# Kernel optimization log

Hardware: AMD Instinct MI355X
Metric: run time of the kernel (lower is better)

## Reference

```python
import jax, jax.numpy as jnp
import numpy as np

N_SRC, N_DST, E, D, H = 100000, 10000, 320000, 128, 128
LN_EPS = 1e-5


def setup_inputs() -> dict:
    key = jax.random.key(0)
    ks = jax.random.split(key, 12)
    h_src = jax.random.normal(ks[0], (N_SRC, D), jnp.float32)
    h_dst = jax.random.normal(ks[1], (N_DST, D), jnp.float32)
    s_emb = jax.random.normal(ks[2], (N_DST, D), jnp.float32)
    edge_weight = jax.random.uniform(ks[3], (E,), jnp.float32)
    src_idx = jax.random.randint(ks[4], (E,), 0, N_SRC)
    dst_idx = jnp.sort(jax.random.randint(ks[5], (E,), 0, N_DST))
    # session_attention: Linear(2D->H, no bias) -> tanh -> Linear(H->1, no bias)
    W1 = jax.random.normal(ks[6], (2 * D, H), jnp.float32) / np.sqrt(2 * D)
    w2 = jax.random.normal(ks[7], (H,), jnp.float32) / np.sqrt(H)
    # output_proj: Linear(2D->D) with bias
    Wo = jax.random.normal(ks[8], (2 * D, D), jnp.float32) / np.sqrt(2 * D)
    bo = jnp.zeros((D,), jnp.float32)
    gamma = jnp.ones((D,), jnp.float32)
    beta = jnp.zeros((D,), jnp.float32)
    return {"h_src": h_src, "h_dst": h_dst, "s_emb": s_emb,
            "edge_weight": edge_weight, "src_idx": src_idx, "dst_idx": dst_idx,
            "W1": W1, "w2": w2, "Wo": Wo, "bo": bo, "gamma": gamma, "beta": beta}


def reference(h_src, h_dst, s_emb, edge_weight, src_idx, dst_idx, W1, w2, Wo, bo, gamma, beta):
    d = h_src.shape[1]
    # concat([h_src[src], s_emb[dst]]) @ W1 == h_src[src] @ W1[:d] + s_emb[dst] @ W1[d:]
    # project per-node first (cheaper than per-edge concat matmul)
    p_src = h_src @ W1[:d]          # [N_src, H]
    p_dst = s_emb @ W1[d:]          # [N_dst, H]
    raw = jnp.tanh(p_src[src_idx] + p_dst[dst_idx]) @ w2   # [E]
    raw = raw * edge_weight
    # edge_softmax: segment softmax over incoming edges of each dst node
    seg_max = jax.ops.segment_max(raw, dst_idx, num_segments=h_dst.shape[0])
    seg_max = jnp.where(jnp.isfinite(seg_max), seg_max, 0.0)  # handle degree-0 dsts
    ex = jnp.exp(raw - seg_max[dst_idx])
    den = jax.ops.segment_sum(ex, dst_idx, num_segments=h_dst.shape[0])
    attn = ex / den[dst_idx]                                 # [E]
    # u_mul_e + sum: weighted gather-scatter aggregation
    h_global = jax.ops.segment_sum(h_src[src_idx] * attn[:, None], dst_idx,
                                   num_segments=h_dst.shape[0])  # [N_dst, D]
    # output_proj on concat([h_dst, h_global])
    out = h_dst @ Wo[:d] + h_global @ Wo[d:] + bo
    # residual + layer norm (dropout = identity in eval)
    x = h_dst + out
    mu = jnp.mean(x, axis=-1, keepdims=True)
    var = jnp.mean((x - mu) ** 2, axis=-1, keepdims=True)
    y = (x - mu) / jnp.sqrt(var + LN_EPS) * gamma + beta
    return (y, attn[:, None])
```

## Files before the change

### kernel.cpp

```cpp
#include <hip/hip_runtime.h>
#include <math.h>

#define D128 128
#define SCAP 1024

typedef unsigned int uint32;
typedef unsigned short ushort_t;
typedef short bf16x8 __attribute__((ext_vector_type(8)));
typedef float f32x4 __attribute__((ext_vector_type(4)));

__device__ __forceinline__ ushort_t bf16_of(float x) {
  uint32 u = __float_as_uint(x);
  return (ushort_t)((u + 0x7fffu + ((u >> 16) & 1u)) >> 16);
}
__device__ __forceinline__ uint32 pack_bf2(float x, float y) {
  uint32 bx = __float_as_uint(x);
  uint32 by = __float_as_uint(y);
  bx = (bx + 0x7fffu + ((bx >> 16) & 1u)) >> 16;
  by = (by + 0x7fffu + ((by >> 16) & 1u)) & 0xffff0000u;
  return bx | by;
}
__device__ __forceinline__ float bf_lo(uint32 u) { return __uint_as_float(u << 16); }
__device__ __forceinline__ float bf_hi(uint32 u) { return __uint_as_float(u & 0xffff0000u); }

__device__ __forceinline__ float fast_tanh(float x) {
  float e = __expf(2.0f * x);
  float r = __builtin_amdgcn_rcpf(1.0f + e);
  return fmaf(-2.0f, r, 1.0f);
}

__global__ __launch_bounds__(256) void prep_all(
    const float* __restrict__ h_src, const float* __restrict__ s_emb,
    const float* __restrict__ h_dst,
    const float* __restrict__ W1, const float* __restrict__ Wo,
    const int* __restrict__ dst_idx,
    uint32* __restrict__ h_src_bf, uint32* __restrict__ s_emb_bf,
    uint32* __restrict__ h_dst_bf,
    ushort_t* __restrict__ Wfrag, ushort_t* __restrict__ Wo_frag,
    int* __restrict__ off,
    int n_src_el, int n_dst_el, int E, int N, int nb_conv) {
  const int b = blockIdx.x;
  const int tid = threadIdx.x;
  if (b < nb_conv) {
    int i = (b * 256 + tid) * 8;
    const int n_tot_el = n_src_el + 2 * n_dst_el;
    if (i >= n_tot_el) return;
    const float* src;
    uint32* dst;
    if (i < n_src_el) { src = h_src + i; dst = h_src_bf + (i >> 1); }
    else if (i < n_src_el + n_dst_el) {
      src = s_emb + (i - n_src_el); dst = s_emb_bf + ((i - n_src_el) >> 1);
    } else {
      src = h_dst + (i - n_src_el - n_dst_el);
      dst = h_dst_bf + ((i - n_src_el - n_dst_el) >> 1);
    }
    float4 a = *(const float4*)src;
    float4 c = *(const float4*)(src + 4);
    uint4 p;
    p.x = pack_bf2(a.x, a.y);
    p.y = pack_bf2(a.z, a.w);
    p.z = pack_bf2(c.x, c.y);
    p.w = pack_bf2(c.z, c.w);
    *(uint4*)dst = p;
  } else if (b < nb_conv + 16) {
    int t = (b - nb_conv) * 256 + tid;
    int lane = t & 63;
    int kc = (t >> 6) & 3;
    int nt = (t >> 8) & 7;
    int h = (t >> 11) & 1;
    int m = lane & 15;
    int quad = lane >> 4;
    int krow = h * D128 + kc * 32 + quad * 8;
    int ncol = nt * 16 + m;
    ushort_t fr[8];
#pragma unroll
    for (int j = 0; j < 8; j++) fr[j] = bf16_of(W1[(size_t)(krow + j) * D128 + ncol]);
    *(uint4*)(Wfrag + (size_t)t * 8) = *(const uint4*)fr;
  } else if (b < nb_conv + 32) {
    int t = (b - nb_conv - 16) * 256 + tid;
    int lane = t & 63;
    int kc = (t >> 6) & 7;
    int nt = (t >> 9) & 7;
    int m = lane & 15;
    int quad = lane >> 4;
    int krow = kc * 32 + quad * 8;
    int ncol = nt * 16 + m;
    ushort_t fr[8];
#pragma unroll
    for (int j = 0; j < 8; j++) fr[j] = bf16_of(Wo[(size_t)(krow + j) * D128 + ncol]);
    *(uint4*)(Wo_frag + (size_t)t * 8) = *(const uint4*)fr;
  } else {
    int e = (b - nb_conv - 32) * 256 + tid;
    if (e >= E) return;
    int d = dst_idx[e];
    int dprev = (e == 0) ? -1 : dst_idx[e - 1];
    for (int v = dprev + 1; v <= d; v++) off[v] = e;
    if (e == E - 1) {
      for (int v = d + 1; v <= N; v++) off[v] = E;
    }
  }
}

__global__ __launch_bounds__(256) void gemm_mfma(
    const ushort_t* __restrict__ Xa, const ushort_t* __restrict__ Xb,
    const ushort_t* __restrict__ Wfrag,
    ushort_t* __restrict__ Pa, ushort_t* __restrict__ Pb,
    int Ma, int Mb, int nblk_a) {
  __shared__ ushort_t Ys[128][132];
  const int blk = blockIdx.x;
  const ushort_t* X;
  const bf16x8* Wf;
  ushort_t* P;
  int M, row0;
  if (blk < nblk_a) { X = Xa; P = Pa; Wf = (const bf16x8*)Wfrag;           M = Ma; row0 = blk * 128; }
  else              { X = Xb; P = Pb; Wf = (const bf16x8*)(Wfrag + 16384); M = Mb; row0 = (blk - nblk_a) * 128; }

  const int tid = threadIdx.x;
  const int wave = tid >> 6;
  const int lane = tid & 63;
  const int m = lane & 15;
  const int quad = lane >> 4;

  const int ra0 = min(row0 + wave * 32 + m, M - 1);
  const int ra1 = min(row0 + wave * 32 + 16 + m, M - 1);

  f32x4 acc[2][8];
#pragma unroll
  for (int st = 0; st < 2; st++)
#pragma unroll
    for (int nt = 0; nt < 8; nt++) acc[st][nt] = (f32x4){0.f, 0.f, 0.f, 0.f};

#pragma unroll
  for (int kc = 0; kc < 4; kc++) {
    bf16x8 a0 = *(const bf16x8*)(X + (size_t)ra0 * D128 + kc * 32 + quad * 8);
    bf16x8 a1 = *(const bf16x8*)(X + (size_t)ra1 * D128 + kc * 32 + quad * 8);
#pragma unroll
    for (int nt = 0; nt < 8; nt++) {
      bf16x8 bfr = Wf[(nt * 4 + kc) * 64 + lane];
      acc[0][nt] = __builtin_amdgcn_mfma_f32_16x16x32_bf16(a0, bfr, acc[0][nt], 0, 0, 0);
      acc[1][nt] = __builtin_amdgcn_mfma_f32_16x16x32_bf16(a1, bfr, acc[1][nt], 0, 0, 0);
    }
  }

#pragma unroll
  for (int st = 0; st < 2; st++)
#pragma unroll
    for (int nt = 0; nt < 8; nt++)
#pragma unroll
      for (int r = 0; r < 4; r++)
        Ys[wave * 32 + st * 16 + quad * 4 + r][nt * 16 + m] = bf16_of(acc[st][nt][r]);
  __syncthreads();

#pragma unroll
  for (int it = 0; it < 16; it++) {
    int f = tid + 256 * it;
    int row = f >> 5;
    int c = (f & 31) * 4;
    int grow = row0 + row;
    if (grow < M) {
      uint2 v = *(const uint2*)(&Ys[row][c]);
      *(uint2*)(P + (size_t)grow * D128 + c) = v;
    }
  }
}

__global__ __launch_bounds__(256) void attn_agg_kernel(
    const uint32* __restrict__ p_src_bf, const uint32* __restrict__ p_dst_bf,
    const float* __restrict__ w2, const float* __restrict__ ew,
    const int* __restrict__ src_idx, const int* __restrict__ off,
    const uint32* __restrict__ h_src_bf2,
    float* __restrict__ attn_out, uint32* __restrict__ h_glob_bf) {
  const int v = blockIdx.x;
  const int tid = threadIdx.x;
  const int lo = off[v], hi = off[v + 1];
  const int deg = hi - lo;
  const int sub = tid & 15;
  const int eg16 = tid >> 4;
  const int t2 = tid & 63;
  const int wv = tid >> 6;

  __shared__ float sw2[128];
  __shared__ uint32 spd[64];
  __shared__ float sred[4];
  __shared__ float sex[SCAP];
  __shared__ int ssrc[SCAP];
  __shared__ float sacc[4][128];

  if (tid < 128) sw2[tid] = w2[tid];
  if (tid < 64) spd[tid] = p_dst_bf[(size_t)v * 64 + tid];
  __syncthreads();

  float accx = 0.f, accy = 0.f;
  float inv;

  if (deg <= SCAP) {
    for (int base = 0; base < deg; base += 16) {
      int ei = base + eg16;
      float acc = 0.f;
      int s = 0;
      if (ei < deg) {
        int e = lo + ei;
        s = src_idx[e];
        uint4 us = *(const uint4*)(p_src_bf + (size_t)s * 64 + sub * 4);
        uint4 ud = *(const uint4*)(&spd[sub * 4]);
        float4 wA = *(const float4*)(&sw2[sub * 8]);
        float4 wB = *(const float4*)(&sw2[sub * 8 + 4]);
        acc = fast_tanh(bf_lo(us.x) + bf_lo(ud.x)) * wA.x;
        acc = fmaf(fast_tanh(bf_hi(us.x) + bf_hi(ud.x)), wA.y, acc);
        acc = fmaf(fast_tanh(bf_lo(us.y) + bf_lo(ud.y)), wA.z, acc);
        acc = fmaf(fast_tanh(bf_hi(us.y) + bf_hi(ud.y)), wA.w, acc);
        acc = fmaf(fast_tanh(bf_lo(us.z) + bf_lo(ud.z)), wB.x, acc);
        acc = fmaf(fast_tanh(bf_hi(us.z) + bf_hi(ud.z)), wB.y, acc);
        acc = fmaf(fast_tanh(bf_lo(us.w) + bf_lo(ud.w)), wB.z, acc);
        acc = fmaf(fast_tanh(bf_hi(us.w) + bf_hi(ud.w)), wB.w, acc);
      }
#pragma unroll
      for (int o = 1; o <= 8; o <<= 1) acc += __shfl_xor(acc, o, 64);
      if (ei < deg && sub == 0) { sex[ei] = acc * ew[lo + ei]; ssrc[ei] = s; }
    }
    const int pad = (deg + 7) & ~7;
    for (int i = deg + tid; i < pad; i += 256) { sex[i] = 0.f; ssrc[i] = 0; }
    __syncthreads();

    float dp = 0.f;
    for (int i = tid; i < deg; i += 256) {
      float ex = __expf(sex[i]);
      sex[i] = ex;
      dp += ex;
    }
#pragma unroll
    for (int o = 32; o >= 1; o >>= 1) dp += __shfl_xor(dp, o, 64);
    if (t2 == 0) sred[wv] = dp;
    __syncthreads();
    inv = (deg > 0) ? 1.0f / (((sred[0] + sred[1]) + (sred[2] + sred[3]))) : 0.0f;

    for (int i = tid; i < deg; i += 256) attn_out[lo + i] = sex[i] * inv;

    const int nb = (deg + 7) >> 3;
    for (int b = wv; b < nb; b += 4) {
      const int base = b * 8;
#pragma unroll
      for (int j = 0; j < 8; j++) {
        float ex = sex[base + j];
        int s = ssrc[base + j];
        uint32 u = h_src_bf2[(size_t)s * 64 + t2];
        accx = fmaf(ex, bf_lo(u), accx);
        accy = fmaf(ex, bf_hi(u), accy);
      }
    }
  } else {
    for (int base = 0; base < deg; base += 16) {
      int ei = base + eg16;
      float acc = 0.f;
      if (ei < deg) {
        int e = lo + ei;
        int s = src_idx[e];
        uint4 us = *(const uint4*)(p_src_bf + (size_t)s * 64 + sub * 4);
        uint4 ud = *(const uint4*)(&spd[sub * 4]);
        float4 wA = *(const float4*)(&sw2[sub * 8]);
        float4 wB = *(const float4*)(&sw2[sub * 8 + 4]);
        acc = fast_tanh(bf_lo(us.x) + bf_lo(ud.x)) * wA.x;
        acc = fmaf(fast_tanh(bf_hi(us.x) + bf_hi(ud.x)), wA.y, acc);
        acc = fmaf(fast_tanh(bf_lo(us.y) + bf_lo(ud.y)), wA.z, acc);
        acc = fmaf(fast_tanh(bf_hi(us.y) + bf_hi(ud.y)), wA.w, acc);
        acc = fmaf(fast_tanh(bf_lo(us.z) + bf_lo(ud.z)), wB.x, acc);
        acc = fmaf(fast_tanh(bf_hi(us.z) + bf_hi(ud.z)), wB.y, acc);
        acc = fmaf(fast_tanh(bf_lo(us.w) + bf_lo(ud.w)), wB.z, acc);
        acc = fmaf(fast_tanh(bf_hi(us.w) + bf_hi(ud.w)), wB.w, acc);
      }
#pragma unroll
      for (int o = 1; o <= 8; o <<= 1) acc += __shfl_xor(acc, o, 64);
      if (ei < deg && sub == 0) attn_out[lo + ei] = acc * ew[lo + ei];
    }
    __syncthreads();

    float dp = 0.f;
    for (int i = tid; i < deg; i += 256) dp += __expf(attn_out[lo + i]);
#pragma unroll
    for (int o = 32; o >= 1; o >>= 1) dp += __shfl_xor(dp, o, 64);
    if (t2 == 0) sred[wv] = dp;
    __syncthreads();
    inv = 1.0f / (((sred[0] + sred[1]) + (sred[2] + sred[3])));

    for (int w0 = 0; w0 < deg; w0 += SCAP) {
      const int wn = min(SCAP, deg - w0);
      __syncthreads();
      for (int i = tid; i < wn; i += 256) {
        float ex = __expf(attn_out[lo + w0 + i]);
        sex[i] = ex;
        ssrc[i] = src_idx[lo + w0 + i];
        attn_out[lo + w0 + i] = ex * inv;
      }
      const int padw = (wn + 7) & ~7;
      for (int i = wn + tid; i < padw; i += 256) { sex[i] = 0.f; ssrc[i] = 0; }
      __syncthreads();
      const int nb = (wn + 7) >> 3;
      for (int b = wv; b < nb; b += 4) {
        const int base = b * 8;
#pragma unroll
        for (int j = 0; j < 8; j++) {
          float ex = sex[base + j];
          int s = ssrc[base + j];
          uint32 u = h_src_bf2[(size_t)s * 64 + t2];
          accx = fmaf(ex, bf_lo(u), accx);
          accy = fmaf(ex, bf_hi(u), accy);
        }
      }
    }
  }

  sacc[wv][t2 * 2] = accx;
  sacc[wv][t2 * 2 + 1] = accy;
  __syncthreads();
  if (tid < 64) {
    float sx = (sacc[0][tid * 2] + sacc[1][tid * 2]) + (sacc[2][tid * 2] + sacc[3][tid * 2]);
    float sy = (sacc[0][tid * 2 + 1] + sacc[1][tid * 2 + 1]) +
               (sacc[2][tid * 2 + 1] + sacc[3][tid * 2 + 1]);
    h_glob_bf[(size_t)v * 64 + tid] = pack_bf2(sx * inv, sy * inv);
  }
}

__global__ __launch_bounds__(128) void out_mfma_ln(
    const ushort_t* __restrict__ h_dst_bf, const ushort_t* __restrict__ h_glob_bf,
    const ushort_t* __restrict__ Wo_frag,
    const float* __restrict__ h_dst, const float* __restrict__ bo,
    const float* __restrict__ gamma, const float* __restrict__ beta,
    float* __restrict__ y, int N) {
  __shared__ float sbo[128], sgam[128], sbet[128];
  const int tid = threadIdx.x;
  if (tid < 128) { sbo[tid] = bo[tid]; sgam[tid] = gamma[tid]; sbet[tid] = beta[tid]; }
  __syncthreads();

  const int w = tid >> 6;
  const int lane = tid & 63;
  const int m = lane & 15;
  const int quad = lane >> 4;
  const int row0 = blockIdx.x * 32 + w * 16;
  const int ra = min(row0 + m, N - 1);
  const bf16x8* Wf = (const bf16x8*)Wo_frag;

  f32x4 acc[8];
#pragma unroll
  for (int nt = 0; nt < 8; nt++) acc[nt] = (f32x4){0.f, 0.f, 0.f, 0.f};

#pragma unroll
  for (int kc = 0; kc < 8; kc++) {
    const ushort_t* X = (kc < 4) ? h_dst_bf : h_glob_bf;
    const int kk = kc & 3;
    bf16x8 a = *(const bf16x8*)(X + (size_t)ra * D128 + kk * 32 + quad * 8);
#pragma unroll
    for (int nt = 0; nt < 8; nt++) {
      bf16x8 bfr = Wf[(nt * 8 + kc) * 64 + lane];
      acc[nt] = __builtin_amdgcn_mfma_f32_16x16x32_bf16(a, bfr, acc[nt], 0, 0, 0);
    }
  }

#pragma unroll
  for (int r = 0; r < 4; r++) {
    const int grow = row0 + quad * 4 + r;
    const int gr = min(grow, N - 1);
    float x[8];
    float s1 = 0.f, s2 = 0.f;
#pragma unroll
    for (int nt = 0; nt < 8; nt++) {
      float hd = h_dst[(size_t)gr * D128 + nt * 16 + m];
      float xv = hd + acc[nt][r] + sbo[nt * 16 + m];
      x[nt] = xv;
      s1 += xv;
      s2 = fmaf(xv, xv, s2);
    }
#pragma unroll
    for (int o = 1; o <= 8; o <<= 1) {
      s1 += __shfl_xor(s1, o, 64);
      s2 += __shfl_xor(s2, o, 64);
    }
    float mu = s1 * (1.0f / 128.0f);
    float var = s2 * (1.0f / 128.0f) - mu * mu;
    float rstd = __builtin_amdgcn_rcpf(sqrtf(var + 1e-5f));
    if (grow < N) {
#pragma unroll
      for (int nt = 0; nt < 8; nt++) {
        int c = nt * 16 + m;
        y[(size_t)grow * D128 + c] = (x[nt] - mu) * rstd * sgam[c] + sbet[c];
      }
    }
  }
}

extern "C" void kernel_launch(void* const* d_in, const int* in_sizes, int n_in,
                              void* d_out, int out_size, void* d_ws, size_t ws_size,
                              hipStream_t stream) {
  const float* h_src = (const float*)d_in[0];
  const float* h_dst = (const float*)d_in[1];
  const float* s_emb = (const float*)d_in[2];
  const float* ew    = (const float*)d_in[3];
  const int* src_idx = (const int*)d_in[4];
  const int* dst_idx = (const int*)d_in[5];
  const float* W1    = (const float*)d_in[6];
  const float* w2    = (const float*)d_in[7];
  const float* Wo    = (const float*)d_in[8];
  const float* bo    = (const float*)d_in[9];
  const float* gamma = (const float*)d_in[10];
  const float* beta  = (const float*)d_in[11];

  const int N_src = in_sizes[0] / D128;
  const int N_dst = in_sizes[1] / D128;
  const int E = in_sizes[3];

  float* out_y = (float*)d_out;
  float* out_attn = out_y + (size_t)N_dst * D128;

  uint32* p_src_bf = (uint32*)d_ws;
  uint32* p_dst_bf = p_src_bf + (size_t)N_src * 64;
  uint32* h_src_bf = p_dst_bf + (size_t)N_dst * 64;
  uint32* h_dst_bf = h_src_bf + (size_t)N_src * 64;
  uint32* h_glob_bf = h_dst_bf + (size_t)N_dst * 64;
  uint32* s_emb_bf = h_glob_bf + (size_t)N_dst * 64;
  int* seg_off = (int*)(s_emb_bf + (size_t)N_dst * 64);
  ushort_t* Wfrag = (ushort_t*)(seg_off + N_dst + 1 + 3);
  ushort_t* Wo_frag = Wfrag + 32768;

  const int n_src_el = N_src * D128;
  const int n_dst_el = N_dst * D128;
  const int n_tot_el = n_src_el + 2 * n_dst_el;
  const int nblk_a = (N_src + 127) / 128;
  const int nblk_b = (N_dst + 127) / 128;
  const int nb_conv = (n_tot_el / 8 + 255) / 256;
  const int nb_seg = (E + 255) / 256;

  prep_all<<<nb_conv + 32 + nb_seg, 256, 0, stream>>>(
      h_src, s_emb, h_dst, W1, Wo, dst_idx,
      h_src_bf, s_emb_bf, h_dst_bf, Wfrag, Wo_frag, seg_off,
      n_src_el, n_dst_el, E, N_dst, nb_conv);
  gemm_mfma<<<nblk_a + nblk_b, 256, 0, stream>>>(
      (const ushort_t*)h_src_bf, (const ushort_t*)s_emb_bf, Wfrag,
      (ushort_t*)p_src_bf, (ushort_t*)p_dst_bf, N_src, N_dst, nblk_a);
  attn_agg_kernel<<<N_dst, 256, 0, stream>>>(
      p_src_bf, p_dst_bf, w2, ew, src_idx, seg_off, h_src_bf, out_attn, h_glob_bf);
  out_mfma_ln<<<(N_dst + 31) / 32, 128, 0, stream>>>(
      (const ushort_t*)h_dst_bf, (const ushort_t*)h_glob_bf, Wo_frag,
      h_dst, bo, gamma, beta, out_y, N_dst);
}
```

Baseline: 177.4 us.

## Map one wavefront per destination node in attention aggregation kernel

Changes the attention/aggregation kernel from one 256-thread block per destination node to one 64-lane wavefront per node, with four nodes per block. All block-level syncs and shared-memory cross-wave reductions are replaced by wave shuffles. The exp is fused into the score loop so the denominator accumulates without a separate pass. With average degree 32, most of a block's threads previously sat idle; the cost is a serial per-wave loop for high-degree nodes and load imbalance between waves in a block.

```diff
diff --git a/kernel.cpp b/kernel.cpp
--- a/kernel.cpp
+++ b/kernel.cpp
@@ -2,7 +2,7 @@
 #include <math.h>
 
 #define D128 128
-#define SCAP 1024
+#define SCAPW 256
 
 typedef unsigned int uint32;
 typedef unsigned short ushort_t;
@@ -169,42 +169,42 @@
     const float* __restrict__ w2, const float* __restrict__ ew,
     const int* __restrict__ src_idx, const int* __restrict__ off,
     const uint32* __restrict__ h_src_bf2,
-    float* __restrict__ attn_out, uint32* __restrict__ h_glob_bf) {
-  const int v = blockIdx.x;
+    float* __restrict__ attn_out, uint32* __restrict__ h_glob_bf, int N_dst) {
   const int tid = threadIdx.x;
+  const int wv = tid >> 6;
+  const int lane = tid & 63;
+  const int v = blockIdx.x * 4 + wv;
+
+  __shared__ float sw2[128];
+  __shared__ float sex[4][SCAPW];
+  __shared__ int ssrc[4][SCAPW];
+
+  if (tid < 128) sw2[tid] = w2[tid];
+  __syncthreads();
+  if (v >= N_dst) return;
+
   const int lo = off[v], hi = off[v + 1];
   const int deg = hi - lo;
-  const int sub = tid & 15;
-  const int eg16 = tid >> 4;
-  const int t2 = tid & 63;
-  const int wv = tid >> 6;
-
-  __shared__ float sw2[128];
-  __shared__ uint32 spd[64];
-  __shared__ float sred[4];
-  __shared__ float sex[SCAP];
-  __shared__ int ssrc[SCAP];
-  __shared__ float sacc[4][128];
-
-  if (tid < 128) sw2[tid] = w2[tid];
-  if (tid < 64) spd[tid] = p_dst_bf[(size_t)v * 64 + tid];
-  __syncthreads();
-
+  const int sub = lane & 15;
+  const int eg = lane >> 4;
+
+  uint4 ud = *(const uint4*)(p_dst_bf + (size_t)v * 64 + sub * 4);
+  float4 wA = *(const float4*)(&sw2[sub * 8]);
+  float4 wB = *(const float4*)(&sw2[sub * 8 + 4]);
+
+  float den = 0.f;
   float accx = 0.f, accy = 0.f;
-  float inv;
-
-  if (deg <= SCAP) {
-    for (int base = 0; base < deg; base += 16) {
-      int ei = base + eg16;
-      float acc = 0.f;
+
+  if (deg <= SCAPW) {
+    for (int base = 0; base < deg; base += 4) {
+      const int ei = base + eg;
+      float acc = 0.f, ewv = 0.f;
       int s = 0;
       if (ei < deg) {
-        int e = lo + ei;
+        const int e = lo + ei;
         s = src_idx[e];
+        ewv = ew[e];
         uint4 us = *(const uint4*)(p_src_bf + (size_t)s * 64 + sub * 4);
-        uint4 ud = *(const uint4*)(&spd[sub * 4]);
-        float4 wA = *(const float4*)(&sw2[sub * 8]);
-        float4 wB = *(const float4*)(&sw2[sub * 8 + 4]);
         acc = fast_tanh(bf_lo(us.x) + bf_lo(ud.x)) * wA.x;
         acc = fmaf(fast_tanh(bf_hi(us.x) + bf_hi(ud.x)), wA.y, acc);
         acc = fmaf(fast_tanh(bf_lo(us.y) + bf_lo(ud.y)), wA.z, acc);
@@ -216,49 +216,43 @@
       }
 #pragma unroll
       for (int o = 1; o <= 8; o <<= 1) acc += __shfl_xor(acc, o, 64);
-      if (ei < deg && sub == 0) { sex[ei] = acc * ew[lo + ei]; ssrc[ei] = s; }
+      float ex = 0.f;
+      if (ei < deg) {
+        ex = __expf(acc * ewv);
+        if (sub == 0) { sex[wv][ei] = ex; ssrc[wv][ei] = s; }
+      }
+      den += (sub == 0) ? ex : 0.f;
     }
     const int pad = (deg + 7) & ~7;
-    for (int i = deg + tid; i < pad; i += 256) { sex[i] = 0.f; ssrc[i] = 0; }
-    __syncthreads();
-
-    float dp = 0.f;
-    for (int i = tid; i < deg; i += 256) {
-      float ex = __expf(sex[i]);
-      sex[i] = ex;
-      dp += ex;
-    }
-#pragma unroll
-    for (int o = 32; o >= 1; o >>= 1) dp += __shfl_xor(dp, o, 64);
-    if (t2 == 0) sred[wv] = dp;
-    __syncthreads();
-    inv = (deg > 0) ? 1.0f / (((sred[0] + sred[1]) + (sred[2] + sred[3]))) : 0.0f;
-
-    for (int i = tid; i < deg; i += 256) attn_out[lo + i] = sex[i] * inv;
-
-    const int nb = (deg + 7) >> 3;
-    for (int b = wv; b < nb; b += 4) {
+    for (int i = deg + lane; i < pad; i += 64) { sex[wv][i] = 0.f; ssrc[wv][i] = 0; }
+#pragma unroll
+    for (int o = 1; o <= 32; o <<= 1) den += __shfl_xor(den, o, 64);
+    const float inv = (deg > 0) ? 1.0f / den : 0.0f;
+
+    for (int i = lane; i < deg; i += 64) attn_out[lo + i] = sex[wv][i] * inv;
+
+    const int nb = pad >> 3;
+    for (int b = 0; b < nb; b++) {
       const int base = b * 8;
 #pragma unroll
       for (int j = 0; j < 8; j++) {
-        float ex = sex[base + j];
-        int s = ssrc[base + j];
-        uint32 u = h_src_bf2[(size_t)s * 64 + t2];
+        float ex = sex[wv][base + j];
+        int s = ssrc[wv][base + j];
+        uint32 u = h_src_bf2[(size_t)s * 64 + lane];
         accx = fmaf(ex, bf_lo(u), accx);
         accy = fmaf(ex, bf_hi(u), accy);
       }
     }
+    h_glob_bf[(size_t)v * 64 + lane] = pack_bf2(accx * inv, accy * inv);
   } else {
-    for (int base = 0; base < deg; base += 16) {
-      int ei = base + eg16;
-      float acc = 0.f;
+    for (int base = 0; base < deg; base += 4) {
+      const int ei = base + eg;
+      float acc = 0.f, ewv = 0.f;
       if (ei < deg) {
-        int e = lo + ei;
+        const int e = lo + ei;
         int s = src_idx[e];
+        ewv = ew[e];
         uint4 us = *(const uint4*)(p_src_bf + (size_t)s * 64 + sub * 4);
-        uint4 ud = *(const uint4*)(&spd[sub * 4]);
-        float4 wA = *(const float4*)(&sw2[sub * 8]);
-        float4 wB = *(const float4*)(&sw2[sub * 8 + 4]);
         acc = fast_tanh(bf_lo(us.x) + bf_lo(ud.x)) * wA.x;
         acc = fmaf(fast_tanh(bf_hi(us.x) + bf_hi(ud.x)), wA.y, acc);
         acc = fmaf(fast_tanh(bf_lo(us.y) + bf_lo(ud.y)), wA.z, acc);
@@ -270,53 +264,31 @@
       }
 #pragma unroll
       for (int o = 1; o <= 8; o <<= 1) acc += __shfl_xor(acc, o, 64);
-      if (ei < deg && sub == 0) attn_out[lo + ei] = acc * ew[lo + ei];
-    }
-    __syncthreads();
-
-    float dp = 0.f;
-    for (int i = tid; i < deg; i += 256) dp += __expf(attn_out[lo + i]);
-#pragma unroll
-    for (int o = 32; o >= 1; o >>= 1) dp += __shfl_xor(dp, o, 64);
-    if (t2 == 0) sred[wv] = dp;
-    __syncthreads();
-    inv = 1.0f / (((sred[0] + sred[1]) + (sred[2] + sred[3])));
-
-    for (int w0 = 0; w0 < deg; w0 += SCAP) {
-      const int wn = min(SCAP, deg - w0);
-      __syncthreads();
-      for (int i = tid; i < wn; i += 256) {
-        float ex = __expf(attn_out[lo + w0 + i]);
-        sex[i] = ex;
-        ssrc[i] = src_idx[lo + w0 + i];
-        attn_out[lo + w0 + i] = ex * inv;
-      }
-      const int padw = (wn + 7) & ~7;
-      for (int i = wn + tid; i < padw; i += 256) { sex[i] = 0.f; ssrc[i] = 0; }
-      __syncthreads();
-      const int nb = (wn + 7) >> 3;
-      for (int b = wv; b < nb; b += 4) {
-        const int base = b * 8;
-#pragma unroll
-        for (int j = 0; j < 8; j++) {
-          float ex = sex[base + j];
-          int s = ssrc[base + j];
-          uint32 u = h_src_bf2[(size_t)s * 64 + t2];
-          accx = fmaf(ex, bf_lo(u), accx);
-          accy = fmaf(ex, bf_hi(u), accy);
-        }
-      }
-    }
-  }
-
-  sacc[wv][t2 * 2] = accx;
-  sacc[wv][t2 * 2 + 1] = accy;
-  __syncthreads();
-  if (tid < 64) {
-    float sx = (sacc[0][tid * 2] + sacc[1][tid * 2]) + (sacc[2][tid * 2] + sacc[3][tid * 2]);
-    float sy = (sacc[0][tid * 2 + 1] + sacc[1][tid * 2 + 1]) +
-               (sacc[2][tid * 2 + 1] + sacc[3][tid * 2 + 1]);
-    h_glob_bf[(size_t)v * 64 + tid] = pack_bf2(sx * inv, sy * inv);
+      float ex = 0.f;
+      if (ei < deg) {
+        ex = __expf(acc * ewv);
+        if (sub == 0) attn_out[lo + ei] = ex;
+      }
+      den += (sub == 0) ? ex : 0.f;
+    }
+#pragma unroll
+    for (int o = 1; o <= 32; o <<= 1) den += __shfl_xor(den, o, 64);
+    const float inv = 1.0f / den;
+
+    for (int i0 = 0; i0 < deg; i0 += 8) {
+#pragma unroll
+      for (int j = 0; j < 8; j++) {
+        const int i = i0 + j;
+        float ex = 0.f;
+        int s = 0;
+        if (i < deg) { ex = attn_out[lo + i]; s = src_idx[lo + i]; }
+        uint32 u = h_src_bf2[(size_t)s * 64 + lane];
+        accx = fmaf(ex, bf_lo(u), accx);
+        accy = fmaf(ex, bf_hi(u), accy);
+        if (i < deg && lane == 0) attn_out[lo + i] = ex * inv;
+      }
+    }
+    h_glob_bf[(size_t)v * 64 + lane] = pack_bf2(accx * inv, accy * inv);
   }
 }
 
@@ -435,8 +407,9 @@
   gemm_mfma<<<nblk_a + nblk_b, 256, 0, stream>>>(
       (const ushort_t*)h_src_bf, (const ushort_t*)s_emb_bf, Wfrag,
       (ushort_t*)p_src_bf, (ushort_t*)p_dst_bf, N_src, N_dst, nblk_a);
-  attn_agg_kernel<<<N_dst, 256, 0, stream>>>(
-      p_src_bf, p_dst_bf, w2, ew, src_idx, seg_off, h_src_bf, out_attn, h_glob_bf);
+  attn_agg_kernel<<<(N_dst + 3) / 4, 256, 0, stream>>>(
+      p_src_bf, p_dst_bf, w2, ew, src_idx, seg_off, h_src_bf, out_attn,
+      h_glob_bf, N_dst);
   out_mfma_ln<<<(N_dst + 31) / 32, 128, 0, stream>>>(
       (const ushort_t*)h_dst_bf, (const ushort_t*)h_glob_bf, Wo_frag,
       h_dst, bo, gamma, beta, out_y, N_dst);
```

New measurement: 176.4 us. About the same (-0.5%).
